# Performance work log

Hardware: AMD Instinct MI355X
Metric: run time of the kernel (lower is better)

Reference implementation:

```python
import jax, jax.numpy as jnp
import numpy as np

N, E, IN, HID, H, C = 10000, 320000, 64, 64, 4, 64
HC = H * C  # 256


def setup_inputs() -> dict:
    key = jax.random.key(0)
    ks = jax.random.split(key, 40)
    ki = iter(range(40))
    def nrm(shape, scale=0.05):
        return jax.random.normal(ks[next(ki)], shape, dtype=jnp.float32) * scale
    inp = {
        "x": jax.random.normal(ks[next(ki)], (N, IN), dtype=jnp.float32),
        "edge_index": jax.random.randint(ks[next(ki)], (2, E), 0, N, dtype=jnp.int64),
        "lin_w": nrm((IN, HID)), "lin_b": nrm((HID,)),
    }
    dims_in = [HID, HC, HC]
    for i, di in enumerate(dims_in):
        inp[f"gat_w{i}"] = nrm((di, HC))
        inp[f"att_src{i}"] = nrm((H, C))
        inp[f"att_dst{i}"] = nrm((H, C))
        inp[f"gat_b{i}"] = nrm((HC,))
        inp[f"ln_g{i}"] = jnp.ones((HC,), jnp.float32)
        inp[f"ln_b{i}"] = jnp.zeros((HC,), jnp.float32)
    inp["ffn_w1"] = nrm((HC, 2 * HID)); inp["ffn_b1"] = nrm((2 * HID,))
    inp["ffn_w2"] = nrm((2 * HID, 64)); inp["ffn_b2"] = nrm((64,))
    return inp


def _layernorm(x, g, b, eps=1e-5):
    m = jnp.mean(x, -1, keepdims=True)
    v = jnp.var(x, -1, keepdims=True)
    return (x - m) * jax.lax.rsqrt(v + eps) * g + b


def _gat(x, src, dst, w, a_src, a_dst, b):
    # PyG GATConv: per-head linear, additive attention, segment softmax over dst
    xl = (x @ w).reshape(-1, H, C)              # [N,H,C]
    e = jax.nn.leaky_relu(jnp.sum(xl * a_src, -1)[src]
                          + jnp.sum(xl * a_dst, -1)[dst], 0.2)  # [E,H]
    emax = jax.ops.segment_max(e, dst, num_segments=N)
    ex = jnp.exp(e - emax[dst])
    alpha = ex / jax.ops.segment_sum(ex, dst, num_segments=N)[dst]
    out = jax.ops.segment_sum(xl[src] * alpha[:, :, None], dst, num_segments=N)
    return out.reshape(-1, HC) + b


def reference(x, edge_index, lin_w, lin_b,
              gat_w0, att_src0, att_dst0, gat_b0, ln_g0, ln_b0,
              gat_w1, att_src1, att_dst1, gat_b1, ln_g1, ln_b1,
              gat_w2, att_src2, att_dst2, gat_b2, ln_g2, ln_b2,
              ffn_w1, ffn_b1, ffn_w2, ffn_b2):
    loops = jnp.arange(N, dtype=edge_index.dtype)
    src = jnp.concatenate([edge_index[0], loops])  # add_self_loops=True
    dst = jnp.concatenate([edge_index[1], loops])
    h = jax.nn.relu(x @ lin_w + lin_b)
    layers = [(gat_w0, att_src0, att_dst0, gat_b0, ln_g0, ln_b0),
              (gat_w1, att_src1, att_dst1, gat_b1, ln_g1, ln_b1),
              (gat_w2, att_src2, att_dst2, gat_b2, ln_g2, ln_b2)]
    for (w, a_s, a_d, b, g, lb) in layers:
        residual = h
        h = jax.nn.elu(_gat(h, src, dst, w, a_s, a_d, b))
        if residual.shape[-1] != h.shape[-1]:
            residual = jnp.pad(residual, ((0, 0), (0, h.shape[-1] - residual.shape[-1])))
        h = _layernorm(h + residual, g, lb)  # dropout is identity in eval mode
    h = jax.nn.relu(h @ ffn_w1 + ffn_b1)
    return h @ ffn_w2 + ffn_b2
```

## Files before the change

kernel.cpp:

```cpp
#include <hip/hip_runtime.h>

#define N_NODES 10000
#define N_EDGES 320000
#define EL (N_EDGES + N_NODES)
#define HC 256
#define CAP 96

using bf16x8 = __attribute__((ext_vector_type(8))) short;
using f32x4  = __attribute__((ext_vector_type(4))) float;

__device__ __forceinline__ float bf2f(unsigned short u) {
  union { unsigned int i; float f; } v; v.i = ((unsigned int)u) << 16; return v.f;
}
__device__ __forceinline__ unsigned short f2bf(float f) {
  union { float f; unsigned int i; } v; v.f = f;
  unsigned int r = (v.i + 0x7FFFu + ((v.i >> 16) & 1u)) >> 16;
  return (unsigned short)r;
}


__device__ __forceinline__ void convw_body(const float* __restrict__ w,
                                           unsigned short* __restrict__ bt,
                                           int K, int idx) {
  int half = K >> 1;
  int col = idx / half;
  int k2 = (idx % half) * 2;
  ushort2 o;
  o.x = f2bf(w[(size_t)k2 * 256 + col]);
  o.y = f2bf(w[(size_t)(k2 + 1) * 256 + col]);
  *(ushort2*)(bt + (size_t)col * K + k2) = o;
}

__global__ __launch_bounds__(256) void prep_kernel(
    int* __restrict__ cnt,
    const float* __restrict__ w0, unsigned short* __restrict__ bt0,
    const float* __restrict__ w1, unsigned short* __restrict__ bt1,
    const float* __restrict__ w2, unsigned short* __restrict__ bt2) {
  int b = blockIdx.x, tid = threadIdx.x;
  if (b < 40) {
    int i = b * 256 + tid;
    if (i < N_NODES) cnt[i] = 0;
  } else if (b < 72) {
    convw_body(w0, bt0, 64, (b - 40) * 256 + tid);
  } else if (b < 200) {
    convw_body(w1, bt1, 256, (b - 72) * 256 + tid);
  } else {
    convw_body(w2, bt2, 256, (b - 200) * 256 + tid);
  }
}


template <int K>
__device__ void mfma_from_lds(const char* ALds, char* Bsw,
                              const unsigned short* __restrict__ Bt,
                              unsigned short* __restrict__ Cb,
                              const float* __restrict__ att_src,
                              const float* __restrict__ att_dst,
                              float* __restrict__ asrc_out, float* __restrict__ adst_out,
                              int row0, int tid) {
  int wave = tid >> 6, lane = tid & 63;
  int r = lane & 15, g = lane >> 4;

  f32x4 acc[4];
#pragma unroll
  for (int i = 0; i < 4; ++i) acc[i] = {0.f, 0.f, 0.f, 0.f};

  for (int k0 = 0; k0 < K; k0 += 64) {
#pragma unroll
    for (int i = 0; i < 8; ++i) {
      int idx = i * 256 + tid;
      int col = idx >> 3;
      int kc8 = idx & 7;
      uint4 v = *(const uint4*)(Bt + (size_t)col * K + k0 + kc8 * 8);
      *(uint4*)(Bsw + ((col * 128 + kc8 * 16) ^ ((col & 7) << 4))) = v;
    }
    __syncthreads();
    const char* Asl = ALds + (k0 >> 6) * 2048;
#pragma unroll
    for (int chunk = 0; chunk < 2; ++chunk) {
      bf16x8 af = *(const bf16x8*)(Asl + ((r * 128 + chunk * 64 + g * 16) ^ ((r & 7) << 4)));
#pragma unroll
      for (int i = 0; i < 4; ++i) {
        int col = (wave * 4 + i) * 16 + r;
        bf16x8 bfr = *(const bf16x8*)(Bsw + ((col * 128 + chunk * 64 + g * 16) ^ ((col & 7) << 4)));
        acc[i] = __builtin_amdgcn_mfma_f32_16x16x32_bf16(af, bfr, acc[i], 0, 0, 0);
      }
    }
    __syncthreads();
  }

  float asv[4], adv[4];
#pragma unroll
  for (int i = 0; i < 4; ++i) {
    int col = (wave * 4 + i) * 16 + r;
    asv[i] = att_src[col];
    adv[i] = att_dst[col];
  }
#pragma unroll
  for (int j = 0; j < 4; ++j) {
    float ps = acc[0][j] * asv[0] + acc[1][j] * asv[1] + acc[2][j] * asv[2] + acc[3][j] * asv[3];
    float pd = acc[0][j] * adv[0] + acc[1][j] * adv[1] + acc[2][j] * adv[2] + acc[3][j] * adv[3];
#pragma unroll
    for (int m = 8; m >= 1; m >>= 1) {
      ps += __shfl_xor(ps, m);
      pd += __shfl_xor(pd, m);
    }
    if (r == 0) {
      int row = row0 + g * 4 + j;
      asrc_out[row * 4 + wave] = ps;
      adst_out[row * 4 + wave] = pd;
    }
  }

#pragma unroll
  for (int i = 0; i < 4; ++i) {
    int col = (wave * 4 + i) * 16 + r;
#pragma unroll
    for (int j = 0; j < 4; ++j) {
      int row = row0 + g * 4 + j;
      Cb[(size_t)row * 256 + col] = f2bf(acc[i][j]);
    }
  }
}


template <int MODE>
__device__ __forceinline__ void agg_node_compute(
    int n, int lane,
    const int* __restrict__ cnt, const int* __restrict__ slots,
    const float* __restrict__ asrc, const float* __restrict__ adst,
    const unsigned short* __restrict__ xb, const float* __restrict__ bias,
    const unsigned short* __restrict__ resid,
    const float* __restrict__ ln_g, const float* __restrict__ ln_b,
    float v[4], int& cbOut) {
  int lh = lane & 31;
  int half = lane >> 5;
  int h = lh >> 3;
  int ch8 = lh << 3;
  float ad = adst[n * 4 + h];

  int i0 = n * CAP;
  int deg = cnt[n];
  int len0 = (deg + 1) >> 1;
  int beg = i0 + (half ? len0 : 0);
  int end = i0 + (half ? deg : len0);
  int last = end - 1;

  float a0 = 0.f, a1 = 0.f, a2 = 0.f, a3 = 0.f, a4 = 0.f, a5 = 0.f, a6 = 0.f, a7 = 0.f;
  float wsum = 0.f;

  int sA[4];
#pragma unroll
  for (int j = 0; j < 4; ++j) sA[j] = slots[min(beg + j, last)];
  float ca[4]; uint4 cx[4];
#pragma unroll
  for (int j = 0; j < 4; ++j) {
    ca[j] = asrc[sA[j] * 4 + h];
    cx[j] = *(const uint4*)(xb + (size_t)sA[j] * HC + ch8);
  }
#pragma unroll
  for (int j = 0; j < 4; ++j) sA[j] = slots[min(beg + 4 + j, last)];

  for (int base = beg; base < end; base += 4) {
    float na[4]; uint4 nx[4];
#pragma unroll
    for (int j = 0; j < 4; ++j) {
      na[j] = asrc[sA[j] * 4 + h];
      nx[j] = *(const uint4*)(xb + (size_t)sA[j] * HC + ch8);
    }
#pragma unroll
    for (int j = 0; j < 4; ++j) sA[j] = slots[min(base + 8 + j, last)];
#pragma unroll
    for (int j = 0; j < 4; ++j) {
      float e = ca[j] + ad;
      e = e > 0.f ? e : 0.2f * e;
      float wg = __expf(e);
      wg = (base + j < end) ? wg : 0.f;
      wsum += wg;
      a0 = fmaf(wg, bf2f((unsigned short)(cx[j].x & 0xffff)), a0);
      a1 = fmaf(wg, bf2f((unsigned short)(cx[j].x >> 16)), a1);
      a2 = fmaf(wg, bf2f((unsigned short)(cx[j].y & 0xffff)), a2);
      a3 = fmaf(wg, bf2f((unsigned short)(cx[j].y >> 16)), a3);
      a4 = fmaf(wg, bf2f((unsigned short)(cx[j].z & 0xffff)), a4);
      a5 = fmaf(wg, bf2f((unsigned short)(cx[j].z >> 16)), a5);
      a6 = fmaf(wg, bf2f((unsigned short)(cx[j].w & 0xffff)), a6);
      a7 = fmaf(wg, bf2f((unsigned short)(cx[j].w >> 16)), a7);
    }
#pragma unroll
    for (int j = 0; j < 4; ++j) { ca[j] = na[j]; cx[j] = nx[j]; }
  }

  a0 += __shfl_xor(a0, 32); a1 += __shfl_xor(a1, 32);
  a2 += __shfl_xor(a2, 32); a3 += __shfl_xor(a3, 32);
  a4 += __shfl_xor(a4, 32); a5 += __shfl_xor(a5, 32);
  a6 += __shfl_xor(a6, 32); a7 += __shfl_xor(a7, 32);
  wsum += __shfl_xor(wsum, 32);

  int cb = ch8 + half * 4;
  float v0 = half ? a4 : a0;
  float v1 = half ? a5 : a1;
  float v2 = half ? a6 : a2;
  float v3 = half ? a7 : a3;

  float rw = 1.f / wsum;
  float4 b4 = *(const float4*)(bias + cb);
  v0 = fmaf(v0, rw, b4.x);
  v1 = fmaf(v1, rw, b4.y);
  v2 = fmaf(v2, rw, b4.z);
  v3 = fmaf(v3, rw, b4.w);
  v0 = v0 > 0.f ? v0 : __expf(v0) - 1.f;
  v1 = v1 > 0.f ? v1 : __expf(v1) - 1.f;
  v2 = v2 > 0.f ? v2 : __expf(v2) - 1.f;
  v3 = v3 > 0.f ? v3 : __expf(v3) - 1.f;

  if constexpr (MODE == 0) {
    if (cb < 64) {
      ushort4 r4 = *(const ushort4*)(resid + (size_t)n * 64 + cb);
      v0 += bf2f(r4.x); v1 += bf2f(r4.y); v2 += bf2f(r4.z); v3 += bf2f(r4.w);
    }
  } else {
    ushort4 r4 = *(const ushort4*)(resid + (size_t)n * HC + cb);
    v0 += bf2f(r4.x); v1 += bf2f(r4.y); v2 += bf2f(r4.z); v3 += bf2f(r4.w);
  }

  float s1 = v0 + v1 + v2 + v3;
  float s2 = v0 * v0 + v1 * v1 + v2 * v2 + v3 * v3;
#pragma unroll
  for (int m = 32; m >= 1; m >>= 1) {
    s1 += __shfl_xor(s1, m);
    s2 += __shfl_xor(s2, m);
  }
  float mean = s1 * (1.f / 256.f);
  float var = s2 * (1.f / 256.f) - mean * mean;
  float inv = rsqrtf(var + 1e-5f);

  float4 g4 = *(const float4*)(ln_g + cb);
  float4 lb4 = *(const float4*)(ln_b + cb);
  v[0] = (v0 - mean) * inv * g4.x + lb4.x;
  v[1] = (v1 - mean) * inv * g4.y + lb4.y;
  v[2] = (v2 - mean) * inv * g4.z + lb4.z;
  v[3] = (v3 - mean) * inv * g4.w + lb4.w;
  cbOut = cb;
}


__global__ __launch_bounds__(256) void scatter_linmfma(
    const int* __restrict__ edges, int* __restrict__ cnt, int* __restrict__ slots,
    const float* __restrict__ x, const float* __restrict__ lin_w,
    const float* __restrict__ lin_b, unsigned short* __restrict__ h0,
    const unsigned short* __restrict__ bt0,
    const float* __restrict__ as0, const float* __restrict__ ad0,
    unsigned short* __restrict__ xbA, float* __restrict__ as4A, float* __restrict__ ad4A) {
  __shared__ __align__(16) char smem[34816];
  int tid = threadIdx.x;
  int b = blockIdx.x;
  if (b < 1290) {
    int e = b * 256 + tid;
    if (e >= EL) return;
    int s, d;
    if (e < N_EDGES) { s = edges[e]; d = edges[N_EDGES + e]; }
    else { s = d = e - N_EDGES; }
    int pos = atomicAdd(&cnt[d], 1);
    slots[d * CAP + pos] = s;
    return;
  }
  int row0 = (b - 1290) * 16;
  int g = tid >> 6, lane = tid & 63;
  {
    float (*As)[36] = (float(*)[36])(smem + 2048);
    float (*Bs)[64] = (float(*)[64])(smem + 2048 + 2304);
    float acc[4] = {0.f, 0.f, 0.f, 0.f};
    for (int k0 = 0; k0 < 64; k0 += 32) {
      if (tid < 128) {
        int r = tid >> 3;
        int kc = (tid & 7) << 2;
        *(float4*)&As[r][kc] = *(const float4*)(x + (size_t)(row0 + r) * 64 + k0 + kc);
      }
#pragma unroll
      for (int i = 0; i < 2; ++i) {
        int fidx = (i * 256 + tid) * 4;
        *(float4*)&Bs[fidx >> 6][fidx & 63] =
            *(const float4*)(lin_w + (size_t)(k0 + (fidx >> 6)) * 64 + (fidx & 63));
      }
      __syncthreads();
#pragma unroll
      for (int kk = 0; kk < 32; kk += 4) {
        float a4[4][4];
#pragma unroll
        for (int rr = 0; rr < 4; ++rr) {
          float4 t = *(const float4*)&As[g * 4 + rr][kk];
          a4[rr][0] = t.x; a4[rr][1] = t.y; a4[rr][2] = t.z; a4[rr][3] = t.w;
        }
#pragma unroll
        for (int u = 0; u < 4; ++u) {
          float bb = Bs[kk + u][lane];
#pragma unroll
          for (int rr = 0; rr < 4; ++rr) acc[rr] = fmaf(a4[rr][u], bb, acc[rr]);
        }
      }
      __syncthreads();
    }
    float bl = lin_b[lane];
#pragma unroll
    for (int rr = 0; rr < 4; ++rr) {
      int r = g * 4 + rr;
      unsigned short hv = f2bf(fmaxf(acc[rr] + bl, 0.f));
      h0[(size_t)(row0 + r) * 64 + lane] = hv;
      *(unsigned short*)(smem + ((r * 128 + lane * 2) ^ ((r & 7) << 4))) = hv;
    }
  }
  __syncthreads();
  mfma_from_lds<64>(smem, smem + 2048, bt0, xbA, as0, ad0, as4A, ad4A, row0, tid);
}


template <int MODE>
__global__ __launch_bounds__(256) void aggmfma_kernel(
    const int* __restrict__ cnt, const int* __restrict__ slots,
    const float* __restrict__ asrcIn, const float* __restrict__ adstIn,
    const unsigned short* __restrict__ xbIn, const float* __restrict__ gbias,
    const unsigned short* __restrict__ resid, const float* __restrict__ ln_g,
    const float* __restrict__ ln_b, unsigned short* __restrict__ hOut,
    const unsigned short* __restrict__ Bt, unsigned short* __restrict__ xbOut,
    const float* __restrict__ att_src, const float* __restrict__ att_dst,
    float* __restrict__ asrcOut, float* __restrict__ adstOut) {
  __shared__ __align__(16) char smem[40960];
  int tid = threadIdx.x;
  int wave = tid >> 6, lane = tid & 63;
  int row0 = blockIdx.x * 16;

  for (int nl = 0; nl < 4; ++nl) {
    int r = wave * 4 + nl;
    int n = row0 + r;
    float v[4]; int cb;
    agg_node_compute<MODE>(n, lane, cnt, slots, asrcIn, adstIn, xbIn, gbias,
                           resid, ln_g, ln_b, v, cb);
    ushort4 o;
    o.x = f2bf(v[0]); o.y = f2bf(v[1]); o.z = f2bf(v[2]); o.w = f2bf(v[3]);
    *(ushort4*)(hOut + (size_t)n * HC + cb) = o;
    *(ushort4*)(smem + (cb >> 6) * 2048 + ((r * 128 + (cb & 63) * 2) ^ ((r & 7) << 4))) = o;
  }
  __syncthreads();
  mfma_from_lds<256>(smem, smem + 8192, Bt, xbOut, att_src, att_dst,
                     asrcOut, adstOut, row0, tid);
}


__global__ __launch_bounds__(256) void aggffn_kernel(
    const int* __restrict__ cnt, const int* __restrict__ slots,
    const float* __restrict__ asrcIn, const float* __restrict__ adstIn,
    const unsigned short* __restrict__ xbIn, const float* __restrict__ gbias,
    const unsigned short* __restrict__ resid, const float* __restrict__ ln_g,
    const float* __restrict__ ln_b,
    const float* __restrict__ w1, const float* __restrict__ b1,
    const float* __restrict__ w2, const float* __restrict__ b2,
    float* __restrict__ out) {
  __shared__ __align__(16) char smem[41216];
  float (*AF)[256] = (float(*)[256])smem;
  float (*Bs)[128] = (float(*)[128])(smem + 16384);
  float (*Ms)[132] = (float(*)[132])(smem + 32768);
  int tid = threadIdx.x;
  int wave = tid >> 6, lane = tid & 63;
  int row0 = blockIdx.x * 16;

  for (int nl = 0; nl < 4; ++nl) {
    int r = wave * 4 + nl;
    int n = row0 + r;
    float v[4]; int cb;
    agg_node_compute<1>(n, lane, cnt, slots, asrcIn, adstIn, xbIn, gbias,
                        resid, ln_g, ln_b, v, cb);
    *(float4*)&AF[r][cb] = make_float4(v[0], v[1], v[2], v[3]);
  }
  __syncthreads();

  int g = wave;
  {
    int colBase = lane * 2;
    float acc[4][2];
#pragma unroll
    for (int r = 0; r < 4; ++r) { acc[r][0] = 0.f; acc[r][1] = 0.f; }
    for (int k0 = 0; k0 < 256; k0 += 32) {
#pragma unroll
      for (int i = 0; i < 4; ++i) {
        int fidx = (i * 256 + tid) * 4;
        *(float4*)&Bs[fidx >> 7][fidx & 127] =
            *(const float4*)(w1 + (size_t)(k0 + (fidx >> 7)) * 128 + (fidx & 127));
      }
      __syncthreads();
#pragma unroll
      for (int kk = 0; kk < 32; kk += 4) {
        float a4[4][4];
#pragma unroll
        for (int rr = 0; rr < 4; ++rr) {
          float4 tv = *(const float4*)&AF[g * 4 + rr][k0 + kk];
          a4[rr][0] = tv.x; a4[rr][1] = tv.y; a4[rr][2] = tv.z; a4[rr][3] = tv.w;
        }
#pragma unroll
        for (int u = 0; u < 4; ++u) {
          float2 b = *(const float2*)&Bs[kk + u][colBase];
#pragma unroll
          for (int rr = 0; rr < 4; ++rr) {
            acc[rr][0] = fmaf(a4[rr][u], b.x, acc[rr][0]);
            acc[rr][1] = fmaf(a4[rr][u], b.y, acc[rr][1]);
          }
        }
      }
      __syncthreads();
    }
    float bb0 = b1[colBase], bb1 = b1[colBase + 1];
#pragma unroll
    for (int rr = 0; rr < 4; ++rr) {
      Ms[g * 4 + rr][colBase]     = fmaxf(acc[rr][0] + bb0, 0.f);
      Ms[g * 4 + rr][colBase + 1] = fmaxf(acc[rr][1] + bb1, 0.f);
    }
  }
  __syncthreads();

  {
    float acc[4] = {0.f, 0.f, 0.f, 0.f};
    for (int k0 = 0; k0 < 128; k0 += 32) {
#pragma unroll
      for (int i = 0; i < 2; ++i) {
        int fidx = (i * 256 + tid) * 4;
        *(float4*)&Bs[fidx >> 6][fidx & 63] =
            *(const float4*)(w2 + (size_t)(k0 + (fidx >> 6)) * 64 + (fidx & 63));
      }
      __syncthreads();
#pragma unroll
      for (int kk = 0; kk < 32; ++kk) {
        float b = Bs[kk][lane];
#pragma unroll
        for (int rr = 0; rr < 4; ++rr)
          acc[rr] = fmaf(Ms[g * 4 + rr][k0 + kk], b, acc[rr]);
      }
      __syncthreads();
    }
    float bb = b2[lane];
#pragma unroll
    for (int rr = 0; rr < 4; ++rr) {
      int row = row0 + g * 4 + rr;
      out[(size_t)row * 64 + lane] = acc[rr] + bb;
    }
  }
}


extern "C" void kernel_launch(void* const* d_in, const int* in_sizes, int n_in,
                              void* d_out, int out_size, void* d_ws, size_t ws_size,
                              hipStream_t stream) {
  (void)in_sizes; (void)n_in; (void)out_size; (void)ws_size;
  const float* x      = (const float*)d_in[0];
  const int*   edges  = (const int*)d_in[1];
  const float* lin_w  = (const float*)d_in[2];
  const float* lin_b  = (const float*)d_in[3];
  const float* gat_w[3] = {(const float*)d_in[4], (const float*)d_in[10], (const float*)d_in[16]};
  const float* att_s[3] = {(const float*)d_in[5], (const float*)d_in[11], (const float*)d_in[17]};
  const float* att_d[3] = {(const float*)d_in[6], (const float*)d_in[12], (const float*)d_in[18]};
  const float* gat_b[3] = {(const float*)d_in[7], (const float*)d_in[13], (const float*)d_in[19]};
  const float* ln_g[3]  = {(const float*)d_in[8], (const float*)d_in[14], (const float*)d_in[20]};
  const float* ln_b[3]  = {(const float*)d_in[9], (const float*)d_in[15], (const float*)d_in[21]};
  const float* ffn_w1 = (const float*)d_in[22];
  const float* ffn_b1 = (const float*)d_in[23];
  const float* ffn_w2 = (const float*)d_in[24];
  const float* ffn_b2 = (const float*)d_in[25];

  char* p = (char*)d_ws;
  auto alloc = [&](size_t bytes) {
    char* q = p;
    p += (bytes + 255) & ~(size_t)255;
    return q;
  };
  int* cnt   = (int*)alloc(N_NODES * 4);
  int* slots = (int*)alloc((size_t)N_NODES * CAP * 4);
  unsigned short* h0 = (unsigned short*)alloc((size_t)N_NODES * 64 * 2);
  unsigned short* hA = (unsigned short*)alloc((size_t)N_NODES * HC * 2);
  unsigned short* hB = (unsigned short*)alloc((size_t)N_NODES * HC * 2);
  unsigned short* xbA = (unsigned short*)alloc((size_t)N_NODES * HC * 2);
  unsigned short* xbB = (unsigned short*)alloc((size_t)N_NODES * HC * 2);
  float* as4A = (float*)alloc((size_t)N_NODES * 16);
  float* ad4A = (float*)alloc((size_t)N_NODES * 16);
  float* as4B = (float*)alloc((size_t)N_NODES * 16);
  float* ad4B = (float*)alloc((size_t)N_NODES * 16);
  unsigned short* bt0 = (unsigned short*)alloc(256 * 64 * 2);
  unsigned short* bt1 = (unsigned short*)alloc(256 * 256 * 2);
  unsigned short* bt2 = (unsigned short*)alloc(256 * 256 * 2);

  const int gblk = N_NODES / 16;

  prep_kernel<<<328, 256, 0, stream>>>(cnt, gat_w[0], bt0, gat_w[1], bt1, gat_w[2], bt2);
  scatter_linmfma<<<1290 + gblk, 256, 0, stream>>>(edges, cnt, slots, x, lin_w, lin_b,
                                                   h0, bt0, att_s[0], att_d[0],
                                                   xbA, as4A, ad4A);
  aggmfma_kernel<0><<<gblk, 256, 0, stream>>>(cnt, slots, as4A, ad4A, xbA, gat_b[0],
                                              h0, ln_g[0], ln_b[0], hA,
                                              bt1, xbB, att_s[1], att_d[1], as4B, ad4B);
  aggmfma_kernel<1><<<gblk, 256, 0, stream>>>(cnt, slots, as4B, ad4B, xbB, gat_b[1],
                                              hA, ln_g[1], ln_b[1], hB,
                                              bt2, xbA, att_s[2], att_d[2], as4A, ad4A);
  aggffn_kernel<<<gblk, 256, 0, stream>>>(cnt, slots, as4A, ad4A, xbA, gat_b[2],
                                          hB, ln_g[2], ln_b[2],
                                          ffn_w1, ffn_b1, ffn_w2, ffn_b2, (float*)d_out);
}
```

Measured before the change: 151.4 us.

## Split final aggregation and FFN into separate kernels

Replaces the fused aggregate+FFN kernel with two kernels: a per-node aggregation kernel (4 nodes per block, 2500 blocks) writing bf16 hidden states to global memory, and an FFN kernel that loads those bf16 rows tile by tile into shared memory. The intent is to raise parallelism and occupancy for the gather-heavy aggregation, which previously ran in 625 blocks with 41KB of shared memory each. The cost is an extra kernel launch, a global round trip for the intermediate activations, and bf16 rounding of the FFN input, which was fp32 before.

```diff
diff --git a/kernel.cpp b/kernel.cpp
--- a/kernel.cpp
+++ b/kernel.cpp
@@ -241,6 +241,24 @@
   v[2] = (v2 - mean) * inv * g4.z + lb4.z;
   v[3] = (v3 - mean) * inv * g4.w + lb4.w;
   cbOut = cb;
+}
+
+
+template <int MODE>
+__global__ __launch_bounds__(256) void agg_kernel(
+    const int* __restrict__ cnt, const int* __restrict__ slots,
+    const float* __restrict__ asrc, const float* __restrict__ adst,
+    const unsigned short* __restrict__ xb, const float* __restrict__ bias,
+    const unsigned short* __restrict__ resid, const float* __restrict__ ln_g,
+    const float* __restrict__ ln_b, unsigned short* __restrict__ hout) {
+  int w = threadIdx.x >> 6, lane = threadIdx.x & 63;
+  int n = blockIdx.x * 4 + w;
+  float v[4]; int cb;
+  agg_node_compute<MODE>(n, lane, cnt, slots, asrc, adst, xb, bias,
+                         resid, ln_g, ln_b, v, cb);
+  ushort4 o;
+  o.x = f2bf(v[0]); o.y = f2bf(v[1]); o.z = f2bf(v[2]); o.w = f2bf(v[3]);
+  *(ushort4*)(hout + (size_t)n * HC + cb) = o;
 }
 
 
@@ -346,40 +364,34 @@
 }
 
 
-__global__ __launch_bounds__(256) void aggffn_kernel(
-    const int* __restrict__ cnt, const int* __restrict__ slots,
-    const float* __restrict__ asrcIn, const float* __restrict__ adstIn,
-    const unsigned short* __restrict__ xbIn, const float* __restrict__ gbias,
-    const unsigned short* __restrict__ resid, const float* __restrict__ ln_g,
-    const float* __restrict__ ln_b,
-    const float* __restrict__ w1, const float* __restrict__ b1,
-    const float* __restrict__ w2, const float* __restrict__ b2,
-    float* __restrict__ out) {
-  __shared__ __align__(16) char smem[41216];
-  float (*AF)[256] = (float(*)[256])smem;
-  float (*Bs)[128] = (float(*)[128])(smem + 16384);
-  float (*Ms)[132] = (float(*)[132])(smem + 32768);
+__global__ __launch_bounds__(256) void ffn_kernel(const unsigned short* __restrict__ A,
+                                                  const float* __restrict__ w1,
+                                                  const float* __restrict__ b1,
+                                                  const float* __restrict__ w2,
+                                                  const float* __restrict__ b2,
+                                                  float* __restrict__ out) {
+  __shared__ float As[16][36];
+  __shared__ float Bs[32][128];
+  __shared__ float Ms[16][132];
   int tid = threadIdx.x;
-  int wave = tid >> 6, lane = tid & 63;
   int row0 = blockIdx.x * 16;
-
-  for (int nl = 0; nl < 4; ++nl) {
-    int r = wave * 4 + nl;
-    int n = row0 + r;
-    float v[4]; int cb;
-    agg_node_compute<1>(n, lane, cnt, slots, asrcIn, adstIn, xbIn, gbias,
-                        resid, ln_g, ln_b, v, cb);
-    *(float4*)&AF[r][cb] = make_float4(v[0], v[1], v[2], v[3]);
-  }
-  __syncthreads();
-
-  int g = wave;
+  int g = tid >> 6, lane = tid & 63;
+
   {
     int colBase = lane * 2;
     float acc[4][2];
 #pragma unroll
     for (int r = 0; r < 4; ++r) { acc[r][0] = 0.f; acc[r][1] = 0.f; }
     for (int k0 = 0; k0 < 256; k0 += 32) {
+      if (tid < 128) {
+        int r = tid >> 3;
+        int kc = (tid & 7) << 2;
+        ushort4 av = *(const ushort4*)(A + (size_t)(row0 + r) * 256 + k0 + kc);
+        As[r][kc]     = bf2f(av.x);
+        As[r][kc + 1] = bf2f(av.y);
+        As[r][kc + 2] = bf2f(av.z);
+        As[r][kc + 3] = bf2f(av.w);
+      }
 #pragma unroll
       for (int i = 0; i < 4; ++i) {
         int fidx = (i * 256 + tid) * 4;
@@ -392,7 +404,7 @@
         float a4[4][4];
 #pragma unroll
         for (int rr = 0; rr < 4; ++rr) {
-          float4 tv = *(const float4*)&AF[g * 4 + rr][k0 + kk];
+          float4 tv = *(const float4*)&As[g * 4 + rr][kk];
           a4[rr][0] = tv.x; a4[rr][1] = tv.y; a4[rr][2] = tv.z; a4[rr][3] = tv.w;
         }
 #pragma unroll
@@ -486,6 +498,7 @@
   unsigned short* bt2 = (unsigned short*)alloc(256 * 256 * 2);
 
   const int gblk = N_NODES / 16;
+  const int nblk = N_NODES / 4;
 
   prep_kernel<<<328, 256, 0, stream>>>(cnt, gat_w[0], bt0, gat_w[1], bt1, gat_w[2], bt2);
   scatter_linmfma<<<1290 + gblk, 256, 0, stream>>>(edges, cnt, slots, x, lin_w, lin_b,
@@ -497,7 +510,7 @@
   aggmfma_kernel<1><<<gblk, 256, 0, stream>>>(cnt, slots, as4B, ad4B, xbB, gat_b[1],
                                               hA, ln_g[1], ln_b[1], hB,
                                               bt2, xbA, att_s[2], att_d[2], as4A, ad4A);
-  aggffn_kernel<<<gblk, 256, 0, stream>>>(cnt, slots, as4A, ad4A, xbA, gat_b[2],
-                                          hB, ln_g[2], ln_b[2],
-                                          ffn_w1, ffn_b1, ffn_w2, ffn_b2, (float*)d_out);
-}
+  agg_kernel<1><<<nblk, 256, 0, stream>>>(cnt, slots, as4A, ad4A, xbA, gat_b[2],
+                                          hB, ln_g[2], ln_b[2], hA);
+  ffn_kernel<<<gblk, 256, 0, stream>>>(hA, ffn_w1, ffn_b1, ffn_w2, ffn_b2, (float*)d_out);
+}
```

Result: no change. 149.1 us (-1.5%).
